# Kernel optimization log

Measured on AMD Instinct MI355X. Metric: run time of the kernel, lower is better.

The kernel has to match this reference:

```python
import jax, jax.numpy as jnp
import numpy as np

B, TQ, TB, C, H, INNER = 4, 4096, 2048, 512, 8, 2048
D = C // H


def _ln(x, g, b, eps=1e-5):
    m = x.mean(-1, keepdims=True)
    v = ((x - m) ** 2).mean(-1, keepdims=True)
    return (x - m) / jnp.sqrt(v + eps) * g + b


def _heads(t):
    b, t_, _ = t.shape
    return t.reshape(b, t_, H, D).transpose(0, 2, 1, 3)  # (B,h,T,d)


def _merge(t):
    b, _, t_, _ = t.shape
    return t.transpose(0, 2, 1, 3).reshape(b, t_, C)


def _lin(x, w, b):
    return x @ w + b


def _forward(x, y0, y1,
             ln1_g, ln1_b, ln2_0_g, ln2_0_b, ln2_1_g, ln2_1_b,
             ln3_g, ln3_b, ln4_g, ln4_b, ln5_g, ln5_b,
             ca_q_w, ca_q_b, ca_k0_w, ca_k0_b, ca_v0_w, ca_v0_b,
             ca_k1_w, ca_k1_b, ca_v1_w, ca_v1_b, ca_p_w, ca_p_b,
             sa_q_w, sa_q_b, sa_k_w, sa_k_b, sa_v_w, sa_v_b, sa_p_w, sa_p_b,
             m1_w1, m1_b1, m1_w2, m1_b2, m2_w1, m2_b1, m2_w2, m2_b2):
    # ---- cross-attention (LinearCrossAttention, accumulate over branches) ----
    xn = _ln(x, ln1_g, ln1_b)
    q = jax.nn.softmax(_heads(_lin(xn, ca_q_w, ca_q_b)), axis=-1)  # (B,h,TQ,d)
    out = q
    branches = [(y0, ln2_0_g, ln2_0_b, ca_k0_w, ca_k0_b, ca_v0_w, ca_v0_b),
                (y1, ln2_1_g, ln2_1_b, ca_k1_w, ca_k1_b, ca_v1_w, ca_v1_b)]
    for yi, g, bb, kw, kb, vw, vb in branches:
        yn = _ln(yi, g, bb)
        k = jax.nn.softmax(_heads(_lin(yn, kw, kb)), axis=-1)  # (B,h,TB,d)
        v = _heads(_lin(yn, vw, vb))
        k_sum = k.sum(axis=-2, keepdims=True)                   # (B,h,1,d)
        d_inv = 1.0 / jnp.clip((q * k_sum).sum(-1, keepdims=True), 1e-9)
        ctx = jnp.einsum('bhtd,bhte->bhde', k, v)               # (B,h,d,d)
        out = out + (q @ ctx) * d_inv
    x = x + _lin(_merge(out), ca_p_w, ca_p_b)

    # ---- MLP 1 ----
    h1 = _lin(_ln(x, ln3_g, ln3_b), m1_w1, m1_b1)
    x = x + _lin(jax.nn.gelu(h1, approximate=False), m1_w2, m1_b2)

    # ---- self-attention (LinearAttention, attn_type='l1') ----
    xn = _ln(x, ln4_g, ln4_b)
    q = jax.nn.softmax(_heads(_lin(xn, sa_q_w, sa_q_b)), axis=-1)
    k = jax.nn.softmax(_heads(_lin(xn, sa_k_w, sa_k_b)), axis=-1)
    v = _heads(_lin(xn, sa_v_w, sa_v_b))
    k_sum = k.sum(axis=-2, keepdims=True)
    d_inv = 1.0 / (q * k_sum).sum(-1, keepdims=True)
    ctx = jnp.einsum('bhtd,bhte->bhde', k, v)
    sa = (q @ ctx) * d_inv + q
    x = x + _lin(_merge(sa), sa_p_w, sa_p_b)

    # ---- MLP 2 ----
    h2 = _lin(_ln(x, ln5_g, ln5_b), m2_w1, m2_b1)
    x = x + _lin(jax.nn.gelu(h2, approximate=False), m2_w2, m2_b2)
    return x


def setup_inputs() -> dict:
    key = jax.random.key(0)
    ks = iter(jax.random.split(key, 64))
    s = 1.0 / np.sqrt(C)
    si = 1.0 / np.sqrt(INNER)

    def lin_p(din, dout, scale):
        return (jax.random.normal(next(ks), (din, dout), jnp.float32) * scale,
                jnp.zeros((dout,), jnp.float32))

    inp = {
        'x': jax.random.normal(next(ks), (B, TQ, C), jnp.float32),
        'y0': jax.random.normal(next(ks), (B, TB, C), jnp.float32),
        'y1': jax.random.normal(next(ks), (B, TB, C), jnp.float32),
    }
    for nm in ['ln1', 'ln2_0', 'ln2_1', 'ln3', 'ln4', 'ln5']:
        inp[nm + '_g'] = jnp.ones((C,), jnp.float32)
        inp[nm + '_b'] = jnp.zeros((C,), jnp.float32)
    for nm in ['ca_q', 'ca_k0', 'ca_v0', 'ca_k1', 'ca_v1', 'ca_p',
               'sa_q', 'sa_k', 'sa_v', 'sa_p']:
        w, b = lin_p(C, C, s)
        inp[nm + '_w'] = w
        inp[nm + '_b'] = b
    for nm in ['m1', 'm2']:
        w1, b1 = lin_p(C, INNER, s)
        w2, b2 = lin_p(INNER, C, si)
        inp[nm + '_w1'], inp[nm + '_b1'] = w1, b1
        inp[nm + '_w2'], inp[nm + '_b2'] = w2, b2
    return inp


def reference(x, y0, y1,
              ln1_g, ln1_b, ln2_0_g, ln2_0_b, ln2_1_g, ln2_1_b,
              ln3_g, ln3_b, ln4_g, ln4_b, ln5_g, ln5_b,
              ca_q_w, ca_q_b, ca_k0_w, ca_k0_b, ca_v0_w, ca_v0_b,
              ca_k1_w, ca_k1_b, ca_v1_w, ca_v1_b, ca_p_w, ca_p_b,
              sa_q_w, sa_q_b, sa_k_w, sa_k_b, sa_v_w, sa_v_b, sa_p_w, sa_p_b,
              m1_w1, m1_b1, m1_w2, m1_b2, m2_w1, m2_b1, m2_w2, m2_b2):
    return _forward(x, y0, y1,
                    ln1_g, ln1_b, ln2_0_g, ln2_0_b, ln2_1_g, ln2_1_b,
                    ln3_g, ln3_b, ln4_g, ln4_b, ln5_g, ln5_b,
                    ca_q_w, ca_q_b, ca_k0_w, ca_k0_b, ca_v0_w, ca_v0_b,
                    ca_k1_w, ca_k1_b, ca_v1_w, ca_v1_b, ca_p_w, ca_p_b,
                    sa_q_w, sa_q_b, sa_k_w, sa_k_b, sa_v_w, sa_v_b, sa_p_w, sa_p_b,
                    m1_w1, m1_b1, m1_w2, m1_b2, m2_w1, m2_b1, m2_w2, m2_b2)
```

## Files before the change

### kernel.cpp

```cpp
#include <hip/hip_runtime.h>
#include <hip/hip_bf16.h>
#include <math.h>

#define NBATCH 4
#define TQD 4096
#define TBD 2048
#define CDIM 512
#define NH 8
#define HD 64
#define NINNER 2048

using short8 = __attribute__((ext_vector_type(8))) short;
using f32x4  = __attribute__((ext_vector_type(4))) float;

__device__ __forceinline__ float b2f(short s) {
  return __uint_as_float(((unsigned)(unsigned short)s) << 16);
}
__device__ __forceinline__ short f2b(float f) {
  unsigned u = __float_as_uint(f);
  return (short)((u + 0x7FFFu + ((u >> 16) & 1u)) >> 16);
}
__device__ __forceinline__ unsigned pk2(float a, float b) {
  float2 t; t.x = a; t.y = b;
  __hip_bfloat162 h = __float22bfloat162_rn(t);
  return *(unsigned*)&h;
}
__device__ __forceinline__ float gelu_fast(float x) {
  float x3 = x * x * x;
  float y2 = 1.5957691216f * (x + 0.044715f * x3);
  float e = __expf(y2);
  return x * e / (e + 1.0f);
}
__device__ __forceinline__ void gload16(const short* g, short* l) {
  __builtin_amdgcn_global_load_lds((const __attribute__((address_space(1))) void*)g,
                                   (__attribute__((address_space(3))) void*)l, 16, 0, 0);
}

__launch_bounds__(256)
__global__ void ln_kernel(const float* __restrict__ x, const float* __restrict__ g,
                          const float* __restrict__ b, short* __restrict__ out)
{
  int r = blockIdx.x;
  int tid = threadIdx.x;
  float2 v = ((const float2*)(x + (size_t)r * CDIM))[tid];
  float s = v.x + v.y, s2 = v.x * v.x + v.y * v.y;
#pragma unroll
  for (int m = 1; m < 64; m <<= 1) { s += __shfl_xor(s, m); s2 += __shfl_xor(s2, m); }
  __shared__ float red[8];
  int wave = tid >> 6;
  if ((tid & 63) == 0) { red[wave] = s; red[4 + wave] = s2; }
  __syncthreads();
  s  = red[0] + red[1] + red[2] + red[3];
  s2 = red[4] + red[5] + red[6] + red[7];
  float mean = s * (1.0f / CDIM);
  float var  = s2 * (1.0f / CDIM) - mean * mean;
  float inv  = rsqrtf(var + 1e-5f);
  float2 gg = ((const float2*)g)[tid];
  float2 bb = ((const float2*)b)[tid];
  short2 o;
  o.x = f2b((v.x - mean) * inv * gg.x + bb.x);
  o.y = f2b((v.y - mean) * inv * gg.y + bb.y);
  *((short2*)(out + (size_t)r * CDIM + 2 * tid)) = o;
}

struct TcvtDesc {
  const float* src[14];
  short* dst[14];
  int K[14], N[14], nblk[14];
};
__launch_bounds__(256)
__global__ void tcvt_all(TcvtDesc d)
{
  int blk = blockIdx.x, wi = 0;
  while (blk >= d.nblk[wi]) { blk -= d.nblk[wi]; wi++; }
  const float* __restrict__ W = d.src[wi];
  short* __restrict__ Wt = d.dst[wi];
  int K = d.K[wi], N = d.N[wi];
  __shared__ float t[32][33];
  int nbk = K >> 5;
  int bk = blk % nbk, bn = blk / nbk;
  int cx = threadIdx.x & 31, cy = threadIdx.x >> 5;
#pragma unroll
  for (int i = 0; i < 4; i++)
    t[cy + 8 * i][cx] = W[(size_t)(bk * 32 + cy + 8 * i) * N + bn * 32 + cx];
  __syncthreads();
#pragma unroll
  for (int i = 0; i < 4; i++)
    Wt[(size_t)(bn * 32 + cy + 8 * i) * K + bk * 32 + cx] = f2b(t[cx][cy + 8 * i]);
}

template<int EPI>
__launch_bounds__(512, 2)
__global__ void gemm256(const short* __restrict__ A, const short* __restrict__ Bt,
                        const float* __restrict__ bias, void* __restrict__ outp,
                        int M, int N, int K, int smLimit)
{
  __shared__ short As[2 * 16384];
  __shared__ short Bs[2 * 16384];
  int tid = threadIdx.x, lane = tid & 63, wave = tid >> 6;
  int l15 = lane & 15, g = lane >> 4;
  int wr = wave >> 2, wn = wave & 3;
  int nbn = N >> 8;
  int per = gridDim.x >> 3;
  int wg = (blockIdx.x & 7) * per + (blockIdx.x >> 3);
  int bm = wg / nbn, bn = wg % nbn;
  f32x4 acc[8][4] = {};

  int asl = ((lane & 7) ^ (lane >> 3)) * 8;
  int bsl = ((lane & 3) ^ ((lane >> 3) & 3)) * 8;
  const short* gA0 = A  + (size_t)(bm * 256 + wave * 16 + (lane >> 3)) * K + asl;
  const short* gB0 = Bt + (size_t)(bn * 256 + wave * 32 + (lane >> 2)) * K + bsl;
  const size_t a1off = (size_t)8 * K;
  const size_t b1off = (size_t)16 * K;
  const size_t ah1   = (size_t)128 * K;
  short* lAbase = As + wave * 1024;
  short* lBbase = Bs + wave * 1024;

  int aswz0 = (g ^ (l15 & 7)) * 8;
  int aswz1 = ((4 + g) ^ (l15 & 7)) * 8;
  int arow  = wr * 8192 + l15 * 64;
  int brow  = (wn * 64 + l15) * 32 + (g ^ ((l15 >> 1) & 3)) * 8;

  short8 af[4], bfr[4];
  int NT = K >> 6;

#define STGA(buf, h, kt) { \
    gload16(gA0 + ((h) ? ah1 : 0) + (kt), lAbase + (buf) * 16384 + (h) * 8192); \
    gload16(gA0 + ((h) ? ah1 : 0) + a1off + (kt), lAbase + (buf) * 16384 + (h) * 8192 + 512); }
#define STGB(buf, kk, kt) { \
    gload16(gB0 + (kt) + (kk) * 32, lBbase + (buf) * 16384 + (kk) * 8192); \
    gload16(gB0 + (kt) + b1off + (kk) * 32, lBbase + (buf) * 16384 + (kk) * 8192 + 512); }
#define RDB(buf, kk) { \
    const short* bp = Bs + (buf) * 16384 + (kk) * 8192 + brow; \
    bfr[0] = *(const short8*)(bp);        bfr[1] = *(const short8*)(bp + 512); \
    bfr[2] = *(const short8*)(bp + 1024); bfr[3] = *(const short8*)(bp + 1536); }
#define RDA(buf, mh, sw) { \
    const short* ap = As + (buf) * 16384 + arow + (mh) * 4096 + (sw); \
    af[0] = *(const short8*)(ap);        af[1] = *(const short8*)(ap + 1024); \
    af[2] = *(const short8*)(ap + 2048); af[3] = *(const short8*)(ap + 3072); }
#define MFMAQ(mh) { \
    __builtin_amdgcn_s_setprio(1); \
    _Pragma("unroll") for (int j = 0; j < 4; j++) \
      _Pragma("unroll") for (int n = 0; n < 4; n++) \
        acc[(mh) * 4 + j][n] = __builtin_amdgcn_mfma_f32_16x16x32_bf16(bfr[n], af[j], acc[(mh) * 4 + j][n], 0, 0, 0); \
    __builtin_amdgcn_s_setprio(0); }

  STGB(0, 0, 0); STGA(0, 0, 0); STGA(0, 1, 0); STGB(0, 1, 0);

  for (int t = 0; t < NT - 1; ++t) {
    int buf = t & 1, nb_ = buf ^ 1;
    int kt = (t + 1) << 6;
    STGB(nb_, 0, kt);
    asm volatile("s_waitcnt vmcnt(4)" ::: "memory");
    __builtin_amdgcn_s_barrier(); __builtin_amdgcn_sched_barrier(0);
    RDB(buf, 0); RDA(buf, 0, aswz0);
    MFMAQ(0);
    STGA(nb_, 0, kt);
    __builtin_amdgcn_s_barrier(); __builtin_amdgcn_sched_barrier(0);
    RDA(buf, 1, aswz0);
    MFMAQ(1);
    STGA(nb_, 1, kt);
    asm volatile("s_waitcnt vmcnt(6)" ::: "memory");
    __builtin_amdgcn_s_barrier(); __builtin_amdgcn_sched_barrier(0);
    RDB(buf, 1); RDA(buf, 0, aswz1);
    MFMAQ(0);
    STGB(nb_, 1, kt);
    __builtin_amdgcn_s_barrier(); __builtin_amdgcn_sched_barrier(0);
    RDA(buf, 1, aswz1);
    MFMAQ(1);
  }
  {
    int buf = (NT - 1) & 1;
    asm volatile("s_waitcnt vmcnt(2)" ::: "memory");
    __builtin_amdgcn_s_barrier(); __builtin_amdgcn_sched_barrier(0);
    RDB(buf, 0); RDA(buf, 0, aswz0); MFMAQ(0);
    RDA(buf, 1, aswz0); MFMAQ(1);
    asm volatile("s_waitcnt vmcnt(0)" ::: "memory");
    __builtin_amdgcn_s_barrier(); __builtin_amdgcn_sched_barrier(0);
    RDB(buf, 1); RDA(buf, 0, aswz1); MFMAQ(0);
    RDA(buf, 1, aswz1); MFMAQ(1);
  }
#undef STGA
#undef STGB
#undef RDB
#undef RDA
#undef MFMAQ

  int row0 = bm * 256 + wr * 128, col0 = bn * 256 + wn * 64;
#pragma unroll
  for (int n = 0; n < 4; n++) {
    f32x4 bz = *(const f32x4*)(bias + col0 + n * 16 + g * 4);
#pragma unroll
    for (int m = 0; m < 8; m++)
#pragma unroll
      for (int r = 0; r < 4; r++) acc[m][n][r] += bz[r];
  }
  if (EPI == 0 && col0 < smLimit) {
#pragma unroll
    for (int m = 0; m < 8; m++) {
      float mx = acc[m][0][0];
#pragma unroll
      for (int n = 0; n < 4; n++)
#pragma unroll
        for (int r = 0; r < 4; r++) mx = fmaxf(mx, acc[m][n][r]);
      mx = fmaxf(mx, __shfl_xor(mx, 16));
      mx = fmaxf(mx, __shfl_xor(mx, 32));
      float s = 0.0f;
#pragma unroll
      for (int n = 0; n < 4; n++)
#pragma unroll
        for (int r = 0; r < 4; r++) {
          float e = __expf(acc[m][n][r] - mx);
          acc[m][n][r] = e; s += e;
        }
      s += __shfl_xor(s, 16);
      s += __shfl_xor(s, 32);
      float inv = 1.0f / s;
#pragma unroll
      for (int n = 0; n < 4; n++)
#pragma unroll
        for (int r = 0; r < 4; r++) acc[m][n][r] *= inv;
    }
  }
  if (EPI == 1) {
#pragma unroll
    for (int m = 0; m < 8; m++)
#pragma unroll
      for (int n = 0; n < 4; n++)
#pragma unroll
        for (int r = 0; r < 4; r++) acc[m][n][r] = gelu_fast(acc[m][n][r]);
  }
#pragma unroll
  for (int m = 0; m < 8; m++) {
    int row = row0 + m * 16 + l15;
#pragma unroll
    for (int n = 0; n < 4; n++) {
      size_t base = (size_t)row * N + col0 + n * 16 + g * 4;
      uint2 u;
      u.x = pk2(acc[m][n][0], acc[m][n][1]);
      u.y = pk2(acc[m][n][2], acc[m][n][3]);
      *(uint2*)((unsigned short*)outp + base) = u;
    }
  }
}

enum { EPI_B_BF16 = 0, EPI_B_RES_F32 = 2 };

template<int EPI>
__launch_bounds__(256)
__global__ void gemm_bt(const short* __restrict__ A, const short* __restrict__ Bt,
                        const float* __restrict__ bias, const float* __restrict__ resid,
                        void* __restrict__ outp, int M, int N, int K, int smLimit)
{
  __shared__ short As[2 * 4096];
  __shared__ short Bs[2 * 4096];
  int tid = threadIdx.x;
  int lane = tid & 63, wave = tid >> 6;
  int l15 = lane & 15, g = lane >> 4;
  int nbn = N >> 7;
  int per = gridDim.x >> 3;
  int wg = (blockIdx.x & 7) * per + (blockIdx.x >> 3);
  int bm = wg / nbn, bn = wg % nbn;
  int wr = wave >> 1, wc = wave & 1;
  f32x4 acc[4][4] = {};

  int srcslot = (lane & 3) ^ ((lane >> 3) & 3);
  const short* gA0 = A  + (size_t)(bm * 128 + wave * 16 + (lane >> 2)) * K + srcslot * 8;
  const short* gB0 = Bt + (size_t)(bn * 128 + wave * 16 + (lane >> 2)) * K + srcslot * 8;
  const short* gA1 = gA0 + (size_t)64 * K;
  const short* gB1 = gB0 + (size_t)64 * K;
  short* lA0 = As + wave * 512;
  short* lA1 = As + wave * 512 + 2048;
  short* lB0 = Bs + wave * 512;
  short* lB1 = Bs + wave * 512 + 2048;
  int rslot = (g ^ ((l15 >> 1) & 3)) * 8;
  const short* ra = As + (wr * 64 + l15) * 32 + rslot;
  const short* rb = Bs + (wc * 64 + l15) * 32 + rslot;

  gload16(gA0, lA0); gload16(gA1, lA1);
  gload16(gB0, lB0); gload16(gB1, lB1);

  int cur = 0;
  for (int kt = 0; kt < K; kt += 32) {
    if (kt + 32 < K) {
      int nb_ = cur ^ 1;
      gload16(gA0 + kt + 32, lA0 + nb_ * 4096);
      gload16(gA1 + kt + 32, lA1 + nb_ * 4096);
      gload16(gB0 + kt + 32, lB0 + nb_ * 4096);
      gload16(gB1 + kt + 32, lB1 + nb_ * 4096);
      asm volatile("s_waitcnt vmcnt(4)" ::: "memory");
    } else {
      asm volatile("s_waitcnt vmcnt(0)" ::: "memory");
    }
    __builtin_amdgcn_s_barrier();
    __builtin_amdgcn_sched_barrier(0);
    const short* rac = ra + cur * 4096;
    const short* rbc = rb + cur * 4096;
    short8 af[4], bfr[4];
#pragma unroll
    for (int m = 0; m < 4; m++) af[m]  = *(const short8*)(rac + m * 512);
#pragma unroll
    for (int n = 0; n < 4; n++) bfr[n] = *(const short8*)(rbc + n * 512);
    __builtin_amdgcn_s_setprio(1);
#pragma unroll
    for (int m = 0; m < 4; m++)
#pragma unroll
      for (int n = 0; n < 4; n++)
        acc[m][n] = __builtin_amdgcn_mfma_f32_16x16x32_bf16(bfr[n], af[m], acc[m][n], 0, 0, 0);
    __builtin_amdgcn_s_setprio(0);
    __builtin_amdgcn_sched_barrier(0);
    __builtin_amdgcn_s_barrier();
    cur ^= 1;
  }

  int row0 = bm * 128 + wr * 64, col0 = bn * 128 + wc * 64;
#pragma unroll
  for (int n = 0; n < 4; n++) {
    f32x4 bz = *(const f32x4*)(bias + col0 + n * 16 + g * 4);
#pragma unroll
    for (int m = 0; m < 4; m++)
#pragma unroll
      for (int r = 0; r < 4; r++)
        acc[m][n][r] += bz[r];
  }
  if (EPI == EPI_B_BF16 && col0 < smLimit) {
#pragma unroll
    for (int m = 0; m < 4; m++) {
      float mx = acc[m][0][0];
#pragma unroll
      for (int n = 0; n < 4; n++)
#pragma unroll
        for (int r = 0; r < 4; r++) mx = fmaxf(mx, acc[m][n][r]);
      mx = fmaxf(mx, __shfl_xor(mx, 16));
      mx = fmaxf(mx, __shfl_xor(mx, 32));
      float s = 0.0f;
#pragma unroll
      for (int n = 0; n < 4; n++)
#pragma unroll
        for (int r = 0; r < 4; r++) {
          float e = __expf(acc[m][n][r] - mx);
          acc[m][n][r] = e; s += e;
        }
      s += __shfl_xor(s, 16);
      s += __shfl_xor(s, 32);
      float inv = 1.0f / s;
#pragma unroll
      for (int n = 0; n < 4; n++)
#pragma unroll
        for (int r = 0; r < 4; r++) acc[m][n][r] *= inv;
    }
  }
#pragma unroll
  for (int m = 0; m < 4; m++) {
    int row = row0 + m * 16 + l15;
#pragma unroll
    for (int n = 0; n < 4; n++) {
      size_t base = (size_t)row * N + col0 + n * 16 + g * 4;
      if (EPI == EPI_B_RES_F32) {
        f32x4 rv = *(const f32x4*)(resid + base);
        f32x4 o;
#pragma unroll
        for (int r = 0; r < 4; r++) o[r] = rv[r] + acc[m][n][r];
        *(f32x4*)((float*)outp + base) = o;
      } else {
        uint2 u;
        u.x = pk2(acc[m][n][0], acc[m][n][1]);
        u.y = pk2(acc[m][n][2], acc[m][n][3]);
        *(uint2*)((unsigned short*)outp + base) = u;
      }
    }
  }
}

#define LDC 40
__launch_bounds__(256)
__global__ void ctx_kernel(const short* __restrict__ k, const short* __restrict__ v,
                           float* __restrict__ ctx, int T, int parts, int SD)
{
  __shared__ short kT[4][64 * LDC];
  __shared__ short vT[4][64 * LDC];
  int bh = blockIdx.x & 31, part = blockIdx.x >> 5;
  int b = bh >> 3, h = bh & 7;
  int tid = threadIdx.x, lane = tid & 63, wave = tid >> 6;
  int l15 = lane & 15, g = lane >> 4;
  int tlen = T / (4 * parts);
  int tbeg = (part * 4 + wave) * tlen;
  f32x4 acc[4][4] = {};
  short* myK = kT[wave];
  short* myV = vT[wave];
  for (int t0 = tbeg; t0 < tbeg + tlen; t0 += 32) {
#pragma unroll
    for (int j = 0; j < 4; j++) {
      int c = lane + j * 64;
      int r = c >> 3, d0 = (c & 7) * 8;
      short8 kv = *(const short8*)(k + (size_t)(b * T + t0 + r) * SD + h * 64 + d0);
      short8 vv = *(const short8*)(v + (size_t)(b * T + t0 + r) * SD + h * 64 + d0);
#pragma unroll
      for (int i = 0; i < 8; i++) {
        myK[(d0 + i) * LDC + r] = kv[i];
        myV[(d0 + i) * LDC + r] = vv[i];
      }
    }
    __syncthreads();
    short8 af[4], bfr[4];
#pragma unroll
    for (int m = 0; m < 4; m++) af[m]  = *(const short8*)(myK + (m * 16 + l15) * LDC + g * 8);
#pragma unroll
    for (int n = 0; n < 4; n++) bfr[n] = *(const short8*)(myV + (n * 16 + l15) * LDC + g * 8);
#pragma unroll
    for (int m = 0; m < 4; m++)
#pragma unroll
      for (int n = 0; n < 4; n++)
        acc[m][n] = __builtin_amdgcn_mfma_f32_16x16x32_bf16(af[m], bfr[n], acc[m][n], 0, 0, 0);
    __syncthreads();
  }
  float* cp = ctx + (size_t)bh * 64 * 64;
#pragma unroll
  for (int m = 0; m < 4; m++)
#pragma unroll
    for (int n = 0; n < 4; n++)
#pragma unroll
      for (int r = 0; r < 4; r++)
        atomicAdd(cp + (m * 16 + g * 4 + r) * 64 + (n * 16 + l15), acc[m][n][r]);
}

__launch_bounds__(256)
__global__ void colsum_kernel(const short* __restrict__ k, float* __restrict__ ksum,
                              int T, int SD)
{
  int part = blockIdx.x & 7, bh = blockIdx.x >> 3;
  int b = bh >> 3, h = bh & 7;
  int d = threadIdx.x & 63, tq = threadIdx.x >> 6;
  int tlen = T >> 3, t0 = part * tlen;
  float s = 0.0f;
  for (int t = t0 + tq; t < t0 + tlen; t += 4)
    s += b2f(k[(size_t)(b * T + t) * SD + h * 64 + d]);
  atomicAdd(&ksum[bh * 64 + d], s);
}

#define LQ 72
__launch_bounds__(256)
__global__ void qctx_kernel(const short* __restrict__ q,
                            const float* __restrict__ ctx,
                            const float* __restrict__ ksum,
                            short* __restrict__ outp, int T, int nb, int SD)
{
  __shared__ short qs[128 * LQ];
  __shared__ short cT[2][64 * LQ];
  __shared__ float dls[2][128];
  int ntb = T >> 7;
  int bh = blockIdx.x / ntb, tq = blockIdx.x % ntb;
  int b = bh >> 3, h = bh & 7;
  int tid = threadIdx.x, lane = tid & 63, wave = tid >> 6;
  int l15 = lane & 15, g = lane >> 4;
  size_t qbase = (size_t)(b * T + tq * 128) * SD + h * 64;
  size_t obase = (size_t)(b * T + tq * 128) * CDIM + h * 64;

#pragma unroll
  for (int j = 0; j < 4; j++) {
    int c = tid + j * 256;
    int r = c >> 3, d0 = (c & 7) * 8;
    *(short8*)(qs + r * LQ + d0) = *(const short8*)(q + qbase + (size_t)r * SD + d0);
  }
  for (int br = 0; br < nb; br++) {
    const float* cp = ctx + ((size_t)br * 32 + bh) * 4096;
#pragma unroll
    for (int j = 0; j < 16; j++) {
      int e2 = tid + j * 256;
      int dd = e2 >> 6, ee = e2 & 63;
      cT[br][ee * LQ + dd] = f2b(cp[e2]);
    }
  }
  __syncthreads();

  int r0 = wave * 32;
  for (int br = 0; br < nb; br++) {
    int row = r0 + (lane >> 1);
    int dbase = (lane & 1) * 32;
    const float* kp = ksum + ((size_t)br * 32 + bh) * 64 + dbase;
    float s = 0.0f;
#pragma unroll
    for (int d = 0; d < 32; d++)
      s += b2f(qs[row * LQ + dbase + d]) * kp[d];
    s += __shfl_xor(s, 1);
    if (!(lane & 1)) dls[br][row] = 1.0f / fmaxf(s, 1e-9f);
  }

  short8 af[2][2];
#pragma unroll
  for (int m = 0; m < 2; m++)
#pragma unroll
    for (int kk = 0; kk < 2; kk++)
      af[m][kk] = *(const short8*)(qs + (r0 + m * 16 + l15) * LQ + kk * 32 + g * 8);

  float ofin[2][4][4];
#pragma unroll
  for (int m = 0; m < 2; m++)
#pragma unroll
    for (int n = 0; n < 4; n++)
#pragma unroll
      for (int r = 0; r < 4; r++)
        ofin[m][n][r] = b2f(qs[(r0 + m * 16 + g * 4 + r) * LQ + n * 16 + l15]);

  for (int br = 0; br < nb; br++) {
    f32x4 acc[2][4] = {};
#pragma unroll
    for (int kk = 0; kk < 2; kk++) {
      short8 bfr[4];
#pragma unroll
      for (int n = 0; n < 4; n++)
        bfr[n] = *(const short8*)(cT[br] + (n * 16 + l15) * LQ + kk * 32 + g * 8);
#pragma unroll
      for (int m = 0; m < 2; m++)
#pragma unroll
        for (int n = 0; n < 4; n++)
          acc[m][n] = __builtin_amdgcn_mfma_f32_16x16x32_bf16(af[m][kk], bfr[n], acc[m][n], 0, 0, 0);
    }
#pragma unroll
    for (int m = 0; m < 2; m++)
#pragma unroll
      for (int n = 0; n < 4; n++)
#pragma unroll
        for (int r = 0; r < 4; r++)
          ofin[m][n][r] += dls[br][r0 + m * 16 + g * 4 + r] * acc[m][n][r];
  }

#pragma unroll
  for (int m = 0; m < 2; m++)
#pragma unroll
    for (int n = 0; n < 4; n++)
#pragma unroll
      for (int r = 0; r < 4; r++) {
        int row = r0 + m * 16 + g * 4 + r;
        int col = n * 16 + l15;
        outp[obase + (size_t)row * CDIM + col] = f2b(ofin[m][n][r]);
      }
}

extern "C" void kernel_launch(void* const* d_in, const int* in_sizes, int n_in,
                              void* d_out, int out_size, void* d_ws, size_t ws_size,
                              hipStream_t stream)
{
  (void)in_sizes; (void)n_in; (void)out_size; (void)ws_size;
  const float* x     = (const float*)d_in[0];
  const float* y0    = (const float*)d_in[1];
  const float* y1    = (const float*)d_in[2];
  const float* ln1g  = (const float*)d_in[3];
  const float* ln1b  = (const float*)d_in[4];
  const float* ln20g = (const float*)d_in[5];
  const float* ln20b = (const float*)d_in[6];
  const float* ln21g = (const float*)d_in[7];
  const float* ln21b = (const float*)d_in[8];
  const float* ln3g  = (const float*)d_in[9];
  const float* ln3b  = (const float*)d_in[10];
  const float* ln4g  = (const float*)d_in[11];
  const float* ln4b  = (const float*)d_in[12];
  const float* ln5g  = (const float*)d_in[13];
  const float* ln5b  = (const float*)d_in[14];
  const float* caqw  = (const float*)d_in[15];
  const float* caqb  = (const float*)d_in[16];
  const float* cak0w = (const float*)d_in[17];
  const float* cak0b = (const float*)d_in[18];
  const float* cav0w = (const float*)d_in[19];
  const float* cav0b = (const float*)d_in[20];
  const float* cak1w = (const float*)d_in[21];
  const float* cak1b = (const float*)d_in[22];
  const float* cav1w = (const float*)d_in[23];
  const float* cav1b = (const float*)d_in[24];
  const float* capw  = (const float*)d_in[25];
  const float* capb  = (const float*)d_in[26];
  const float* saqw  = (const float*)d_in[27];
  const float* saqb  = (const float*)d_in[28];
  const float* sakw  = (const float*)d_in[29];
  const float* sakb  = (const float*)d_in[30];
  const float* savw  = (const float*)d_in[31];
  const float* savb  = (const float*)d_in[32];
  const float* sapw  = (const float*)d_in[33];
  const float* sapb  = (const float*)d_in[34];
  const float* m1w1  = (const float*)d_in[35];
  const float* m1b1  = (const float*)d_in[36];
  const float* m1w2  = (const float*)d_in[37];
  const float* m1b2  = (const float*)d_in[38];
  const float* m2w1  = (const float*)d_in[39];
  const float* m2b1  = (const float*)d_in[40];
  const float* m2w2  = (const float*)d_in[41];
  const float* m2b2  = (const float*)d_in[42];
  float* xout = (float*)d_out;

  char* p = (char*)d_ws;
  size_t off = 0;
  auto take = [&](size_t bytes) {
    char* r = p + off;
    off += (bytes + 255) & ~(size_t)255;
    return r;
  };
  const size_t W512 = (size_t)512 * 512 * 2;
  const size_t WMLP = (size_t)2048 * 512 * 2;
  short* wt_caq   = (short*)take(W512);
  short* wt_cakv0 = (short*)take(2 * W512);
  short* wt_cakv1 = (short*)take(2 * W512);
  short* wt_cap   = (short*)take(W512);
  short* wt_saqkv = (short*)take(3 * W512);
  short* wt_sap   = (short*)take(W512);
  short* wt_m1w1  = (short*)take(WMLP);
  short* wt_m1w2  = (short*)take(WMLP);
  short* wt_m2w1  = (short*)take(WMLP);
  short* wt_m2w2  = (short*)take(WMLP);
  float* b_saqkv  = (float*)take(1536 * 4);
  float* b_cakv0  = (float*)take(1024 * 4);
  float* b_cakv1  = (float*)take(1024 * 4);
  short* xn   = (short*)take((size_t)16384 * 512 * 2);
  short* bufD = (short*)take((size_t)16384 * 512 * 2);
  short* big  = (short*)take((size_t)16384 * 1536 * 2);
  short* h1   = (short*)take((size_t)16384 * 2048 * 2);
  float* ksum = (float*)take((size_t)2 * 32 * 64 * 4);
  float* ctxb = (float*)take((size_t)2 * 32 * 64 * 64 * 4);

  short* q_ca  = big;
  short* kv_ca = big + (size_t)8 * 1024 * 1024;
  short* qkv   = big;

  const int MQ  = NBATCH * TQD;
  const int MKV = NBATCH * TBD;

  {
    TcvtDesc d;
    const float* srcs[14] = {caqw, cak0w, cav0w, cak1w, cav1w, capw,
                             saqw, sakw, savw, sapw, m1w1, m1w2, m2w1, m2w2};
    short* dsts[14] = {wt_caq, wt_cakv0, wt_cakv0 + 512 * 512,
                       wt_cakv1, wt_cakv1 + 512 * 512, wt_cap,
                       wt_saqkv, wt_saqkv + 512 * 512, wt_saqkv + 2 * 512 * 512, wt_sap,
                       wt_m1w1, wt_m1w2, wt_m2w1, wt_m2w2};
    int Ks[14] = {512,512,512,512,512,512,512,512,512,512, 512,2048,512,2048};
    int Ns[14] = {512,512,512,512,512,512,512,512,512,512, 2048,512,2048,512};
    int total = 0;
    for (int i = 0; i < 14; i++) {
      d.src[i] = srcs[i]; d.dst[i] = dsts[i]; d.K[i] = Ks[i]; d.N[i] = Ns[i];
      d.nblk[i] = (Ks[i] >> 5) * (Ns[i] >> 5);
      total += d.nblk[i];
    }
    tcvt_all<<<total, 256, 0, stream>>>(d);
  }
  hipMemcpyAsync(b_saqkv,        saqb,  512 * 4, hipMemcpyDeviceToDevice, stream);
  hipMemcpyAsync(b_saqkv + 512,  sakb,  512 * 4, hipMemcpyDeviceToDevice, stream);
  hipMemcpyAsync(b_saqkv + 1024, savb,  512 * 4, hipMemcpyDeviceToDevice, stream);
  hipMemcpyAsync(b_cakv0,        cak0b, 512 * 4, hipMemcpyDeviceToDevice, stream);
  hipMemcpyAsync(b_cakv0 + 512,  cav0b, 512 * 4, hipMemcpyDeviceToDevice, stream);
  hipMemcpyAsync(b_cakv1,        cak1b, 512 * 4, hipMemcpyDeviceToDevice, stream);
  hipMemcpyAsync(b_cakv1 + 512,  cav1b, 512 * 4, hipMemcpyDeviceToDevice, stream);

  ln_kernel<<<MQ, 256, 0, stream>>>(x, ln1g, ln1b, xn);
  gemm_bt<0><<<512, 256, 0, stream>>>(xn, wt_caq, caqb, nullptr, q_ca, MQ, 512, 512, 512);
  hipMemsetAsync(ksum, 0, (size_t)2 * 32 * 64 * 4, stream);
  hipMemsetAsync(ctxb, 0, (size_t)2 * 32 * 64 * 64 * 4, stream);
  for (int br = 0; br < 2; br++) {
    const float* yy = br ? y1 : y0;
    const float* lg = br ? ln21g : ln20g;
    const float* lb = br ? ln21b : ln20b;
    const short* wk = br ? wt_cakv1 : wt_cakv0;
    const float* bk = br ? b_cakv1 : b_cakv0;
    ln_kernel<<<MKV, 256, 0, stream>>>(yy, lg, lb, bufD);
    gemm_bt<0><<<512, 256, 0, stream>>>(bufD, wk, bk, nullptr, kv_ca, MKV, 1024, 512, 512);
    colsum_kernel<<<256, 256, 0, stream>>>(kv_ca, ksum + (size_t)br * 2048, TBD, 1024);
    ctx_kernel<<<256, 256, 0, stream>>>(kv_ca, kv_ca + 512,
                                        ctxb + (size_t)br * 32 * 4096, TBD, 8, 1024);
  }
  qctx_kernel<<<32 * (TQD / 128), 256, 0, stream>>>(q_ca, ctxb, ksum, bufD, TQD, 2, 512);
  gemm_bt<2><<<512, 256, 0, stream>>>(bufD, wt_cap, capb, x, xout, MQ, 512, 512, 0);

  ln_kernel<<<MQ, 256, 0, stream>>>(xout, ln3g, ln3b, xn);
  gemm256<1><<<512, 512, 0, stream>>>(xn, wt_m1w1, m1b1, h1, MQ, 2048, 512, 0);
  gemm_bt<2><<<512, 256, 0, stream>>>(h1, wt_m1w2, m1b2, xout, xout, MQ, 512, 2048, 0);

  ln_kernel<<<MQ, 256, 0, stream>>>(xout, ln4g, ln4b, xn);
  gemm256<0><<<384, 512, 0, stream>>>(xn, wt_saqkv, b_saqkv, qkv, MQ, 1536, 512, 1024);
  hipMemsetAsync(ksum, 0, (size_t)32 * 64 * 4, stream);
  hipMemsetAsync(ctxb, 0, (size_t)32 * 64 * 64 * 4, stream);
  colsum_kernel<<<256, 256, 0, stream>>>(qkv + 512, ksum, TQD, 1536);
  ctx_kernel<<<256, 256, 0, stream>>>(qkv + 512, qkv + 1024, ctxb, TQD, 8, 1536);
  qctx_kernel<<<32 * (TQD / 128), 256, 0, stream>>>(qkv, ctxb, ksum, bufD, TQD, 1, 1536);
  gemm_bt<2><<<512, 256, 0, stream>>>(bufD, wt_sap, sapb, xout, xout, MQ, 512, 512, 0);

  ln_kernel<<<MQ, 256, 0, stream>>>(xout, ln5g, ln5b, xn);
  gemm256<1><<<512, 512, 0, stream>>>(xn, wt_m2w1, m2b1, h1, MQ, 2048, 512, 0);
  gemm_bt<2><<<512, 256, 0, stream>>>(h1, wt_m2w2, m2b2, xout, xout, MQ, 512, 2048, 0);
}
```

Before: 656.0 us.

## Replace 128-tile GEMMs with rescheduled 256-tile GEMM across all projections

Rewrites the 256x256 GEMM main loop to process two K-tiles per iteration, split into quarter-tile MFMA phases with finer barriers and prefetch interleaving. It adds a residual-add fp32 epilogue so the 256 kernel can replace the removed 128x128 gemm_bt kernel for the q, kv, projection and MLP-down GEMMs. N=512 GEMMs now launch only 128 workgroups, which may underfill the 256 CUs while trading for more data reuse per tile.

```diff
diff --git a/kernel.cpp b/kernel.cpp
--- a/kernel.cpp
+++ b/kernel.cpp
@@ -92,8 +92,8 @@
 template<int EPI>
 __launch_bounds__(512, 2)
 __global__ void gemm256(const short* __restrict__ A, const short* __restrict__ Bt,
-                        const float* __restrict__ bias, void* __restrict__ outp,
-                        int M, int N, int K, int smLimit)
+                        const float* __restrict__ bias, const float* __restrict__ resid,
+                        void* __restrict__ outp, int M, int N, int K, int smLimit)
 {
   __shared__ short As[2 * 16384];
   __shared__ short Bs[2 * 16384];
@@ -113,78 +113,85 @@
   const size_t a1off = (size_t)8 * K;
   const size_t b1off = (size_t)16 * K;
   const size_t ah1   = (size_t)128 * K;
-  short* lAbase = As + wave * 1024;
-  short* lBbase = Bs + wave * 1024;
-
-  int aswz0 = (g ^ (l15 & 7)) * 8;
-  int aswz1 = ((4 + g) ^ (l15 & 7)) * 8;
-  int arow  = wr * 8192 + l15 * 64;
-  int brow  = (wn * 64 + l15) * 32 + (g ^ ((l15 >> 1) & 3)) * 8;
-
-  short8 af[4], bfr[4];
-  int NT = K >> 6;
-
-#define STGA(buf, h, kt) { \
-    gload16(gA0 + ((h) ? ah1 : 0) + (kt), lAbase + (buf) * 16384 + (h) * 8192); \
-    gload16(gA0 + ((h) ? ah1 : 0) + a1off + (kt), lAbase + (buf) * 16384 + (h) * 8192 + 512); }
-#define STGB(buf, kk, kt) { \
-    gload16(gB0 + (kt) + (kk) * 32, lBbase + (buf) * 16384 + (kk) * 8192); \
-    gload16(gB0 + (kt) + b1off + (kk) * 32, lBbase + (buf) * 16384 + (kk) * 8192 + 512); }
-#define RDB(buf, kk) { \
-    const short* bp = Bs + (buf) * 16384 + (kk) * 8192 + brow; \
-    bfr[0] = *(const short8*)(bp);        bfr[1] = *(const short8*)(bp + 512); \
-    bfr[2] = *(const short8*)(bp + 1024); bfr[3] = *(const short8*)(bp + 1536); }
-#define RDA(buf, mh, sw) { \
-    const short* ap = As + (buf) * 16384 + arow + (mh) * 4096 + (sw); \
-    af[0] = *(const short8*)(ap);        af[1] = *(const short8*)(ap + 1024); \
-    af[2] = *(const short8*)(ap + 2048); af[3] = *(const short8*)(ap + 3072); }
-#define MFMAQ(mh) { \
+  short* lA = As + wave * 1024;
+  short* lB = Bs + wave * 1024;
+
+  int asw0 = (g ^ (l15 & 7)) * 8;
+  int asw1 = ((4 + g) ^ (l15 & 7)) * 8;
+  const short* raB = As + wr * 8192 + l15 * 64;
+  const short* rbB = Bs + (wn * 64 + l15) * 32 + (g ^ ((l15 >> 1) & 3)) * 8;
+
+  short8 af[4], bfr[8];
+  int NT = K >> 6, NIT = NT >> 1;
+
+#define STGA(T, h) { \
+    const short* s_ = gA0 + (h) * ah1 + (size_t)(T) * 64; \
+    short* d_ = lA + ((T) & 1) * 16384 + (h) * 8192; \
+    gload16(s_, d_); gload16(s_ + a1off, d_ + 512); }
+#define STGB(T, kk) { \
+    const short* s_ = gB0 + (size_t)(T) * 64 + (kk) * 32; \
+    short* d_ = lB + ((T) & 1) * 16384 + (kk) * 8192; \
+    gload16(s_, d_); gload16(s_ + b1off, d_ + 512); }
+#define RDB(T) { \
+    const short* bp = rbB + ((T) & 1) * 16384; \
+    bfr[0] = *(const short8*)(bp);               bfr[1] = *(const short8*)(bp + 512); \
+    bfr[2] = *(const short8*)(bp + 1024);        bfr[3] = *(const short8*)(bp + 1536); \
+    bfr[4] = *(const short8*)(bp + 8192);        bfr[5] = *(const short8*)(bp + 8192 + 512); \
+    bfr[6] = *(const short8*)(bp + 8192 + 1024); bfr[7] = *(const short8*)(bp + 8192 + 1536); }
+#define RDA(T, q) { \
+    const short* ap = raB + ((T) & 1) * 16384 + (q) * 2048; \
+    af[0] = *(const short8*)(ap + asw0); af[1] = *(const short8*)(ap + 1024 + asw0); \
+    af[2] = *(const short8*)(ap + asw1); af[3] = *(const short8*)(ap + 1024 + asw1); }
+#define MFMAQ(q) { \
     __builtin_amdgcn_s_setprio(1); \
-    _Pragma("unroll") for (int j = 0; j < 4; j++) \
-      _Pragma("unroll") for (int n = 0; n < 4; n++) \
-        acc[(mh) * 4 + j][n] = __builtin_amdgcn_mfma_f32_16x16x32_bf16(bfr[n], af[j], acc[(mh) * 4 + j][n], 0, 0, 0); \
+    _Pragma("unroll") for (int n = 0; n < 4; n++) { \
+      acc[2*(q)][n]   = __builtin_amdgcn_mfma_f32_16x16x32_bf16(bfr[n], af[0], acc[2*(q)][n], 0, 0, 0); \
+      acc[2*(q)+1][n] = __builtin_amdgcn_mfma_f32_16x16x32_bf16(bfr[n], af[1], acc[2*(q)+1][n], 0, 0, 0); } \
+    _Pragma("unroll") for (int n = 0; n < 4; n++) { \
+      acc[2*(q)][n]   = __builtin_amdgcn_mfma_f32_16x16x32_bf16(bfr[4+n], af[2], acc[2*(q)][n], 0, 0, 0); \
+      acc[2*(q)+1][n] = __builtin_amdgcn_mfma_f32_16x16x32_bf16(bfr[4+n], af[3], acc[2*(q)+1][n], 0, 0, 0); } \
     __builtin_amdgcn_s_setprio(0); }
-
-  STGB(0, 0, 0); STGA(0, 0, 0); STGA(0, 1, 0); STGB(0, 1, 0);
-
-  for (int t = 0; t < NT - 1; ++t) {
-    int buf = t & 1, nb_ = buf ^ 1;
-    int kt = (t + 1) << 6;
-    STGB(nb_, 0, kt);
-    asm volatile("s_waitcnt vmcnt(4)" ::: "memory");
-    __builtin_amdgcn_s_barrier(); __builtin_amdgcn_sched_barrier(0);
-    RDB(buf, 0); RDA(buf, 0, aswz0);
-    MFMAQ(0);
-    STGA(nb_, 0, kt);
-    __builtin_amdgcn_s_barrier(); __builtin_amdgcn_sched_barrier(0);
-    RDA(buf, 1, aswz0);
-    MFMAQ(1);
-    STGA(nb_, 1, kt);
-    asm volatile("s_waitcnt vmcnt(6)" ::: "memory");
-    __builtin_amdgcn_s_barrier(); __builtin_amdgcn_sched_barrier(0);
-    RDB(buf, 1); RDA(buf, 0, aswz1);
-    MFMAQ(0);
-    STGB(nb_, 1, kt);
-    __builtin_amdgcn_s_barrier(); __builtin_amdgcn_sched_barrier(0);
-    RDA(buf, 1, aswz1);
-    MFMAQ(1);
+#define BARX  { __builtin_amdgcn_s_barrier(); __builtin_amdgcn_sched_barrier(0); }
+#define BAR2  { __builtin_amdgcn_s_barrier(); }
+#define VMW(n) asm volatile("s_waitcnt vmcnt(" #n ")" ::: "memory");
+
+  STGB(0, 0); STGB(0, 1); STGA(0, 0); STGA(0, 1); STGB(1, 0); STGB(1, 1);
+  VMW(4);
+  BAR2;
+
+  for (int t = 0; t < NIT - 1; ++t) {
+    int E = 2 * t, O = 2 * t + 1;
+    RDB(E); RDA(E, 0); STGA(O, 0);     BARX; MFMAQ(0); BAR2;
+    RDA(E, 1);         STGA(O, 1);     BARX; MFMAQ(1); BAR2;
+    RDA(E, 2);         STGB(E + 2, 0); BARX; MFMAQ(2); BAR2;
+    VMW(2);
+    RDA(E, 3);         STGB(E + 2, 1); BARX; MFMAQ(3); BAR2;
+    RDB(O); RDA(O, 0); STGA(E + 2, 0); BARX; MFMAQ(0); BAR2;
+    RDA(O, 1);         STGA(E + 2, 1); BARX; MFMAQ(1); BAR2;
+    RDA(O, 2);         STGB(O + 2, 0); BARX; MFMAQ(2); BAR2;
+    VMW(2);
+    RDA(O, 3);         STGB(O + 2, 1); BARX; MFMAQ(3); BAR2;
   }
   {
-    int buf = (NT - 1) & 1;
-    asm volatile("s_waitcnt vmcnt(2)" ::: "memory");
-    __builtin_amdgcn_s_barrier(); __builtin_amdgcn_sched_barrier(0);
-    RDB(buf, 0); RDA(buf, 0, aswz0); MFMAQ(0);
-    RDA(buf, 1, aswz0); MFMAQ(1);
-    asm volatile("s_waitcnt vmcnt(0)" ::: "memory");
-    __builtin_amdgcn_s_barrier(); __builtin_amdgcn_sched_barrier(0);
-    RDB(buf, 1); RDA(buf, 0, aswz1); MFMAQ(0);
-    RDA(buf, 1, aswz1); MFMAQ(1);
+    int E = NT - 2, O = NT - 1;
+    RDB(E); RDA(E, 0); STGA(O, 0); BARX; MFMAQ(0); BAR2;
+    RDA(E, 1);         STGA(O, 1); BARX; MFMAQ(1); BAR2;
+    RDA(E, 2);                     BARX; MFMAQ(2); BAR2;
+    VMW(0);
+    RDA(E, 3);                     BARX; MFMAQ(3); BAR2;
+    RDB(O); RDA(O, 0);             BARX; MFMAQ(0); BAR2;
+    RDA(O, 1);                     BARX; MFMAQ(1); BAR2;
+    RDA(O, 2);                     BARX; MFMAQ(2); BAR2;
+    RDA(O, 3);                     BARX; MFMAQ(3);
   }
 #undef STGA
 #undef STGB
 #undef RDB
 #undef RDA
 #undef MFMAQ
+#undef BARX
+#undef BAR2
+#undef VMW
 
   int row0 = bm * 256 + wr * 128, col0 = bn * 256 + wn * 64;
 #pragma unroll
@@ -236,127 +243,7 @@
 #pragma unroll
     for (int n = 0; n < 4; n++) {
       size_t base = (size_t)row * N + col0 + n * 16 + g * 4;
-      uint2 u;
-      u.x = pk2(acc[m][n][0], acc[m][n][1]);
-      u.y = pk2(acc[m][n][2], acc[m][n][3]);
-      *(uint2*)((unsigned short*)outp + base) = u;
-    }
-  }
-}
-
-enum { EPI_B_BF16 = 0, EPI_B_RES_F32 = 2 };
-
-template<int EPI>
-__launch_bounds__(256)
-__global__ void gemm_bt(const short* __restrict__ A, const short* __restrict__ Bt,
-                        const float* __restrict__ bias, const float* __restrict__ resid,
-                        void* __restrict__ outp, int M, int N, int K, int smLimit)
-{
-  __shared__ short As[2 * 4096];
-  __shared__ short Bs[2 * 4096];
-  int tid = threadIdx.x;
-  int lane = tid & 63, wave = tid >> 6;
-  int l15 = lane & 15, g = lane >> 4;
-  int nbn = N >> 7;
-  int per = gridDim.x >> 3;
-  int wg = (blockIdx.x & 7) * per + (blockIdx.x >> 3);
-  int bm = wg / nbn, bn = wg % nbn;
-  int wr = wave >> 1, wc = wave & 1;
-  f32x4 acc[4][4] = {};
-
-  int srcslot = (lane & 3) ^ ((lane >> 3) & 3);
-  const short* gA0 = A  + (size_t)(bm * 128 + wave * 16 + (lane >> 2)) * K + srcslot * 8;
-  const short* gB0 = Bt + (size_t)(bn * 128 + wave * 16 + (lane >> 2)) * K + srcslot * 8;
-  const short* gA1 = gA0 + (size_t)64 * K;
-  const short* gB1 = gB0 + (size_t)64 * K;
-  short* lA0 = As + wave * 512;
-  short* lA1 = As + wave * 512 + 2048;
-  short* lB0 = Bs + wave * 512;
-  short* lB1 = Bs + wave * 512 + 2048;
-  int rslot = (g ^ ((l15 >> 1) & 3)) * 8;
-  const short* ra = As + (wr * 64 + l15) * 32 + rslot;
-  const short* rb = Bs + (wc * 64 + l15) * 32 + rslot;
-
-  gload16(gA0, lA0); gload16(gA1, lA1);
-  gload16(gB0, lB0); gload16(gB1, lB1);
-
-  int cur = 0;
-  for (int kt = 0; kt < K; kt += 32) {
-    if (kt + 32 < K) {
-      int nb_ = cur ^ 1;
-      gload16(gA0 + kt + 32, lA0 + nb_ * 4096);
-      gload16(gA1 + kt + 32, lA1 + nb_ * 4096);
-      gload16(gB0 + kt + 32, lB0 + nb_ * 4096);
-      gload16(gB1 + kt + 32, lB1 + nb_ * 4096);
-      asm volatile("s_waitcnt vmcnt(4)" ::: "memory");
-    } else {
-      asm volatile("s_waitcnt vmcnt(0)" ::: "memory");
-    }
-    __builtin_amdgcn_s_barrier();
-    __builtin_amdgcn_sched_barrier(0);
-    const short* rac = ra + cur * 4096;
-    const short* rbc = rb + cur * 4096;
-    short8 af[4], bfr[4];
-#pragma unroll
-    for (int m = 0; m < 4; m++) af[m]  = *(const short8*)(rac + m * 512);
-#pragma unroll
-    for (int n = 0; n < 4; n++) bfr[n] = *(const short8*)(rbc + n * 512);
-    __builtin_amdgcn_s_setprio(1);
-#pragma unroll
-    for (int m = 0; m < 4; m++)
-#pragma unroll
-      for (int n = 0; n < 4; n++)
-        acc[m][n] = __builtin_amdgcn_mfma_f32_16x16x32_bf16(bfr[n], af[m], acc[m][n], 0, 0, 0);
-    __builtin_amdgcn_s_setprio(0);
-    __builtin_amdgcn_sched_barrier(0);
-    __builtin_amdgcn_s_barrier();
-    cur ^= 1;
-  }
-
-  int row0 = bm * 128 + wr * 64, col0 = bn * 128 + wc * 64;
-#pragma unroll
-  for (int n = 0; n < 4; n++) {
-    f32x4 bz = *(const f32x4*)(bias + col0 + n * 16 + g * 4);
-#pragma unroll
-    for (int m = 0; m < 4; m++)
-#pragma unroll
-      for (int r = 0; r < 4; r++)
-        acc[m][n][r] += bz[r];
-  }
-  if (EPI == EPI_B_BF16 && col0 < smLimit) {
-#pragma unroll
-    for (int m = 0; m < 4; m++) {
-      float mx = acc[m][0][0];
-#pragma unroll
-      for (int n = 0; n < 4; n++)
-#pragma unroll
-        for (int r = 0; r < 4; r++) mx = fmaxf(mx, acc[m][n][r]);
-      mx = fmaxf(mx, __shfl_xor(mx, 16));
-      mx = fmaxf(mx, __shfl_xor(mx, 32));
-      float s = 0.0f;
-#pragma unroll
-      for (int n = 0; n < 4; n++)
-#pragma unroll
-        for (int r = 0; r < 4; r++) {
-          float e = __expf(acc[m][n][r] - mx);
-          acc[m][n][r] = e; s += e;
-        }
-      s += __shfl_xor(s, 16);
-      s += __shfl_xor(s, 32);
-      float inv = 1.0f / s;
-#pragma unroll
-      for (int n = 0; n < 4; n++)
-#pragma unroll
-        for (int r = 0; r < 4; r++) acc[m][n][r] *= inv;
-    }
-  }
-#pragma unroll
-  for (int m = 0; m < 4; m++) {
-    int row = row0 + m * 16 + l15;
-#pragma unroll
-    for (int n = 0; n < 4; n++) {
-      size_t base = (size_t)row * N + col0 + n * 16 + g * 4;
-      if (EPI == EPI_B_RES_F32) {
+      if (EPI == 2) {
         f32x4 rv = *(const f32x4*)(resid + base);
         f32x4 o;
 #pragma unroll
@@ -650,7 +537,7 @@
   hipMemcpyAsync(b_cakv1 + 512,  cav1b, 512 * 4, hipMemcpyDeviceToDevice, stream);
 
   ln_kernel<<<MQ, 256, 0, stream>>>(x, ln1g, ln1b, xn);
-  gemm_bt<0><<<512, 256, 0, stream>>>(xn, wt_caq, caqb, nullptr, q_ca, MQ, 512, 512, 512);
+  gemm256<0><<<128, 512, 0, stream>>>(xn, wt_caq, caqb, nullptr, q_ca, MQ, 512, 512, 512);
   hipMemsetAsync(ksum, 0, (size_t)2 * 32 * 64 * 4, stream);
   hipMemsetAsync(ctxb, 0, (size_t)2 * 32 * 64 * 64 * 4, stream);
   for (int br = 0; br < 2; br++) {
@@ -660,28 +547,28 @@
     const short* wk = br ? wt_cakv1 : wt_cakv0;
     const float* bk = br ? b_cakv1 : b_cakv0;
     ln_kernel<<<MKV, 256, 0, stream>>>(yy, lg, lb, bufD);
-    gemm_bt<0><<<512, 256, 0, stream>>>(bufD, wk, bk, nullptr, kv_ca, MKV, 1024, 512, 512);
+    gemm256<0><<<128, 512, 0, stream>>>(bufD, wk, bk, nullptr, kv_ca, MKV, 1024, 512, 512);
     colsum_kernel<<<256, 256, 0, stream>>>(kv_ca, ksum + (size_t)br * 2048, TBD, 1024);
     ctx_kernel<<<256, 256, 0, stream>>>(kv_ca, kv_ca + 512,
                                         ctxb + (size_t)br * 32 * 4096, TBD, 8, 1024);
   }
   qctx_kernel<<<32 * (TQD / 128), 256, 0, stream>>>(q_ca, ctxb, ksum, bufD, TQD, 2, 512);
-  gemm_bt<2><<<512, 256, 0, stream>>>(bufD, wt_cap, capb, x, xout, MQ, 512, 512, 0);
+  gemm256<2><<<128, 512, 0, stream>>>(bufD, wt_cap, capb, x, xout, MQ, 512, 512, 0);
 
   ln_kernel<<<MQ, 256, 0, stream>>>(xout, ln3g, ln3b, xn);
-  gemm256<1><<<512, 512, 0, stream>>>(xn, wt_m1w1, m1b1, h1, MQ, 2048, 512, 0);
-  gemm_bt<2><<<512, 256, 0, stream>>>(h1, wt_m1w2, m1b2, xout, xout, MQ, 512, 2048, 0);
+  gemm256<1><<<512, 512, 0, stream>>>(xn, wt_m1w1, m1b1, nullptr, h1, MQ, 2048, 512, 0);
+  gemm256<2><<<128, 512, 0, stream>>>(h1, wt_m1w2, m1b2, xout, xout, MQ, 512, 2048, 0);
 
   ln_kernel<<<MQ, 256, 0, stream>>>(xout, ln4g, ln4b, xn);
-  gemm256<0><<<384, 512, 0, stream>>>(xn, wt_saqkv, b_saqkv, qkv, MQ, 1536, 512, 1024);
+  gemm256<0><<<384, 512, 0, stream>>>(xn, wt_saqkv, b_saqkv, nullptr, qkv, MQ, 1536, 512, 1024);
   hipMemsetAsync(ksum, 0, (size_t)32 * 64 * 4, stream);
   hipMemsetAsync(ctxb, 0, (size_t)32 * 64 * 64 * 4, stream);
   colsum_kernel<<<256, 256, 0, stream>>>(qkv + 512, ksum, TQD, 1536);
   ctx_kernel<<<256, 256, 0, stream>>>(qkv + 512, qkv + 1024, ctxb, TQD, 8, 1536);
   qctx_kernel<<<32 * (TQD / 128), 256, 0, stream>>>(qkv, ctxb, ksum, bufD, TQD, 1, 1536);
-  gemm_bt<2><<<512, 256, 0, stream>>>(bufD, wt_sap, sapb, xout, xout, MQ, 512, 512, 0);
+  gemm256<2><<<128, 512, 0, stream>>>(bufD, wt_sap, sapb, xout, xout, MQ, 512, 512, 0);
 
   ln_kernel<<<MQ, 256, 0, stream>>>(xout, ln5g, ln5b, xn);
-  gemm256<1><<<512, 512, 0, stream>>>(xn, wt_m2w1, m2b1, h1, MQ, 2048, 512, 0);
-  gemm_bt<2><<<512, 256, 0, stream>>>(h1, wt_m2w2, m2b2, xout, xout, MQ, 512, 2048, 0);
-}
+  gemm256<1><<<512, 512, 0, stream>>>(xn, wt_m2w1, m2b1, nullptr, h1, MQ, 2048, 512, 0);
+  gemm256<2><<<128, 512, 0, stream>>>(h1, wt_m2w2, m2b2, xout, xout, MQ, 512, 2048, 0);
+}
```

After: 717.4 us. 1.09x slower.
